# Kernel tuning notes

Hardware: AMD Instinct MI355X
Metric: run time of the kernel (lower is better)

The kernel has to match this reference:

```python
import jax, jax.numpy as jnp
import numpy as np

B = 2          # batch
S = 4096       # byte-level sequence length
D = 512        # d_hidden_bytelevel
BPL = 4        # bytes_per_latent
H = 16         # n_attention_heads
DQK = 64       # d_qkv_bytelevel (== rope d_hidden)
DLAT = 1024    # d_hidden_latent
LQ = S // BPL  # latent sequence length
EPS = 1.1920929e-07  # torch RMSNorm default eps = float32 finfo eps
ROPE_BASE = 10000.0


def _rope(x, pos):
    # x: [B, H, L, DQK], pos: [L] float positions. Half-split rotation.
    half = DQK // 2
    inv_freq = ROPE_BASE ** (-jnp.arange(half, dtype=jnp.float32) / half)  # [half]
    ang = pos[:, None] * inv_freq[None, :]                                 # [L, half]
    cos, sin = jnp.cos(ang), jnp.sin(ang)
    x1, x2 = x[..., :half], x[..., half:]
    return jnp.concatenate([x1 * cos - x2 * sin, x1 * sin + x2 * cos], axis=-1)


def setup_inputs() -> dict:
    key = jax.random.key(0)
    ks = jax.random.split(key, 9)
    s = 0.02
    return {
        "x": jax.random.normal(ks[0], (B, S, D), dtype=jnp.float32),
        "norm_w": jnp.ones((D,), dtype=jnp.float32),
        "wq_w": jax.random.normal(ks[1], (BPL * D, H * DQK), dtype=jnp.float32) * s,
        "wq_b": jax.random.normal(ks[2], (H * DQK,), dtype=jnp.float32) * s,
        "wkv_w": jax.random.normal(ks[3], (D, 2 * H * DQK), dtype=jnp.float32) * s,
        "wkv_b": jax.random.normal(ks[4], (2 * H * DQK,), dtype=jnp.float32) * s,
        "wout_w": jax.random.normal(ks[5], (H * DQK, DLAT), dtype=jnp.float32) * s,
        "wout_b": jax.random.normal(ks[6], (DLAT,), dtype=jnp.float32) * s,
        "wbyp_w": jax.random.normal(ks[7], (BPL * D, DLAT), dtype=jnp.float32) * s,
    }


def reference(x, norm_w, wq_w, wq_b, wkv_w, wkv_b, wout_w, wout_b, wbyp_w):
    # RMSNorm (elementwise affine)
    normalized = x * jax.lax.rsqrt(jnp.mean(x * x, axis=-1, keepdims=True) + EPS) * norm_w
    # merge groups of BPL bytes -> latent query tokens: [B, LQ, BPL*D]
    merged = normalized.reshape(B, LQ, BPL * D)
    # fused Q projection: [B, H, LQ, DQK]
    q = (merged @ wq_w + wq_b).reshape(B, LQ, H, DQK).transpose(0, 2, 1, 3)
    # merged KV projection: split dim first, then heads -> [B, S, 2, H, DQK]
    kv = (normalized @ wkv_w + wkv_b).reshape(B, S, 2, H, DQK)
    k = kv[:, :, 0].transpose(0, 2, 1, 3)  # [B, H, S, DQK]
    v = kv[:, :, 1].transpose(0, 2, 1, 3)
    # strided RoPE for Q (positions i*BPL), unit-stride for K
    q = _rope(q, jnp.arange(LQ, dtype=jnp.float32) * BPL)
    k = _rope(k, jnp.arange(S, dtype=jnp.float32))
    # SDPA (non-causal)
    scores = jnp.einsum('bhqd,bhkd->bhqk', q, k) * (1.0 / np.sqrt(DQK).astype(np.float32))
    attn = jax.nn.softmax(scores, axis=-1)
    attn_out = jnp.einsum('bhqk,bhkd->bhqd', attn, v)
    attn_concat = attn_out.transpose(0, 2, 1, 3).reshape(B, LQ, H * DQK)
    out = attn_concat @ wout_w + wout_b
    # bypass: raw x grouped by BPL, bias-free projection
    bypass = x.reshape(B, LQ, BPL * D) @ wbyp_w
    return out + bypass
```

## Files before the change

kernel.cpp:

```cpp
#include <hip/hip_runtime.h>

using u16 = unsigned short;
using u32 = unsigned int;

typedef __attribute__((ext_vector_type(8))) short bf16x8;
typedef __attribute__((ext_vector_type(8))) unsigned short u16x8;
typedef __attribute__((ext_vector_type(4))) float f32x4;
typedef __attribute__((ext_vector_type(16))) float f32x16;
typedef __attribute__((ext_vector_type(4))) u32 u32x4;

constexpr int Bb   = 2;
constexpr int Ss   = 4096;
constexpr int Dd   = 512;
constexpr int Hh   = 16;
constexpr int DQK  = 64;
constexpr int LQ   = 1024;
constexpr int DLAT = 1024;

#define QSCL 0.18033688011112042f

__device__ __forceinline__ u16 f2bf(float f){
  u32 u = __float_as_uint(f);
  u += 0x7FFFu + ((u >> 16) & 1u);
  return (u16)(u >> 16);
}
__device__ __forceinline__ u32 permpack(float hi, float lo){
  return __builtin_amdgcn_perm(__float_as_uint(hi), __float_as_uint(lo), 0x07060302u);
}

#define GLDS16(gp, lp) \
  __builtin_amdgcn_global_load_lds((const __attribute__((address_space(1))) u32*)(gp), \
                                   (__attribute__((address_space(3))) u32*)(lp), 16, 0, 0)

__global__ __launch_bounds__(256) void rmsnorm_kernel(
    const float* __restrict__ x, const float* __restrict__ w,
    u16* __restrict__ normb, u16* __restrict__ xb)
{
  const int lane = threadIdx.x & 63;
  const int row  = blockIdx.x * 4 + (threadIdx.x >> 6);
  const float4* xr = (const float4*)(x + (size_t)row * Dd);
  float4 a = xr[lane*2], b2 = xr[lane*2 + 1];
  float ss = a.x*a.x + a.y*a.y + a.z*a.z + a.w*a.w
           + b2.x*b2.x + b2.y*b2.y + b2.z*b2.z + b2.w*b2.w;
  #pragma unroll
  for (int off = 1; off < 64; off <<= 1) ss += __shfl_xor(ss, off);
  const float sc = rsqrtf(ss * (1.0f / Dd) + 1.1920929e-07f);
  const int c0 = lane * 8;
  const float4* wr4 = (const float4*)(w + c0);
  float4 w0 = wr4[0], w1 = wr4[1];
  u16x8 nv, xv;
  nv[0]=f2bf(a.x *sc*w0.x); nv[1]=f2bf(a.y *sc*w0.y); nv[2]=f2bf(a.z *sc*w0.z); nv[3]=f2bf(a.w *sc*w0.w);
  nv[4]=f2bf(b2.x*sc*w1.x); nv[5]=f2bf(b2.y*sc*w1.y); nv[6]=f2bf(b2.z*sc*w1.z); nv[7]=f2bf(b2.w*sc*w1.w);
  xv[0]=f2bf(a.x);  xv[1]=f2bf(a.y);  xv[2]=f2bf(a.z);  xv[3]=f2bf(a.w);
  xv[4]=f2bf(b2.x); xv[5]=f2bf(b2.y); xv[6]=f2bf(b2.z); xv[7]=f2bf(b2.w);
  *(u16x8*)(normb + (size_t)row * Dd + c0) = nv;
  *(u16x8*)(xb    + (size_t)row * Dd + c0) = xv;
}

__global__ __launch_bounds__(256) void rope_tab_kernel(float2* __restrict__ tab){
  int i = blockIdx.x * 256 + threadIdx.x;
  int pos = i >> 5, d = i & 31;
  float inv = exp2f(-(float)d * 0.41524101186092028f);
  float ang = (float)pos * inv;
  float s, c;
  sincosf(ang, &s, &c);
  tab[i] = make_float2(c, s);
}

__global__ __launch_bounds__(256) void transpose_cast_kernel(
    const float* __restrict__ W, u16* __restrict__ Wt,
    int N, int ldt, int koff)
{
  __shared__ float t[64][65];
  const int k0 = blockIdx.x * 64, n0 = blockIdx.y * 64;
  const int c = threadIdx.x & 63, r0 = threadIdx.x >> 6;
  #pragma unroll
  for (int i = 0; i < 16; ++i){
    int r = i*4 + r0;
    t[r][c] = W[(size_t)(k0 + r) * N + n0 + c];
  }
  __syncthreads();
  #pragma unroll
  for (int i = 0; i < 16; ++i){
    int r = i*4 + r0;
    Wt[(size_t)(n0 + r) * ldt + koff + k0 + c] = f2bf(t[c][r]);
  }
}

__device__ __forceinline__ void gemm_core64(
    const u16* __restrict__ A, int lda,
    const u16* __restrict__ Bt, int ldb, int kofs,
    int K, int bm0, int bn0, char* lds,
    f32x4 (&acc)[4])
{
  const int tid = threadIdx.x, lane = tid & 63, w = tid >> 6;
  const int l15 = lane & 15, l4 = lane >> 4;

  #pragma unroll
  for (int j = 0; j < 4; ++j) acc[j] = (f32x4){0.f, 0.f, 0.f, 0.f};

  auto stage = [&](int t){
    char* dst = lds + (t % 3) * 16384;
    const int k0 = t * 64;
    #pragma unroll
    for (int i = 0; i < 4; ++i){
      int u = i*256 + tid;
      int row = u >> 3;
      int colb = ((u & 7) * 16) ^ ((row & 7) << 4);
      const u16* src = (row < 64)
        ? A  + (size_t)(bm0 + row) * lda + k0 + (colb >> 1)
        : Bt + (size_t)(bn0 + row - 64) * ldb + kofs + k0 + (colb >> 1);
      GLDS16(src, dst + u*16);
    }
  };

  const int nt = K >> 6;
  stage(0);
  if (nt > 1) stage(1);

  #pragma unroll 1
  for (int t = 0; t < nt; ++t){
    if (t + 1 < nt) { asm volatile("s_waitcnt vmcnt(4)" ::: "memory"); }
    else            { asm volatile("s_waitcnt vmcnt(0)" ::: "memory"); }
    __builtin_amdgcn_sched_barrier(0);
    __builtin_amdgcn_s_barrier();

    const char* kb = lds + (t % 3) * 16384;
    bf16x8 af[2], bf[4][2];
    #pragma unroll
    for (int ks = 0; ks < 2; ++ks){
      const int row = w*16 + l15;
      af[ks] = *(const bf16x8*)(kb + row*128 + ((ks*64 + l4*16) ^ ((row & 7) << 4)));
    }
    #pragma unroll
    for (int j = 0; j < 4; ++j)
      #pragma unroll
      for (int ks = 0; ks < 2; ++ks){
        const int row = 64 + j*16 + l15;
        bf[j][ks] = *(const bf16x8*)(kb + row*128 + ((ks*64 + l4*16) ^ ((row & 7) << 4)));
      }
    asm volatile("s_waitcnt lgkmcnt(0)" ::: "memory");
    __builtin_amdgcn_sched_barrier(0);
    if (t + 2 < nt) stage(t + 2);

    __builtin_amdgcn_s_setprio(1);
    #pragma unroll
    for (int ks = 0; ks < 2; ++ks)
      #pragma unroll
      for (int j = 0; j < 4; ++j)
        acc[j] = __builtin_amdgcn_mfma_f32_16x16x32_bf16(af[ks], bf[j][ks], acc[j], 0, 0, 0);
    __builtin_amdgcn_s_setprio(0);
  }
}

__global__ __launch_bounds__(256, 3) void qkv_kernel(
    const u16* __restrict__ normb,
    const u16* __restrict__ wtq, const u16* __restrict__ wtkv,
    const float* __restrict__ wq_b, const float* __restrict__ wkv_b,
    const float2* __restrict__ rtab,
    u16* __restrict__ Qb, u16* __restrict__ Kb, u16* __restrict__ Vtb)
{
  __shared__ char lds[49152];
  const int bid = blockIdx.x;
  const int lane = threadIdx.x & 63, w = threadIdx.x >> 6;
  const int ml = (lane >> 4) * 4, nl = lane & 15;
  f32x4 acc[4];

  if (bid < 512){
    const int bm0 = (bid & 31) * 64, bn0 = (bid >> 5) * 64;
    gemm_core64(normb, 2048, wtq, 2048, 0, 2048, bm0, bn0, lds, acc);
    const int h = bn0 >> 6;
    #pragma unroll
    for (int j = 0; j < 2; ++j){
      const int d1 = j*16 + nl;
      const float b1 = wq_b[bn0 + j*16 + nl], b2v = wq_b[bn0 + (j+2)*16 + nl];
      #pragma unroll
      for (int r = 0; r < 4; ++r){
        int m = bm0 + w*16 + ml + r;
        int b = m >> 10, lq = m & 1023;
        float x1 = acc[j][r] + b1;
        float x2 = acc[j+2][r] + b2v;
        float2 cs = rtab[(lq*4)*32 + d1];
        size_t ob = ((size_t)(b*Hh + h) * LQ + lq) * DQK;
        Qb[ob + d1]      = f2bf((x1*cs.x - x2*cs.y) * QSCL);
        Qb[ob + d1 + 32] = f2bf((x1*cs.y + x2*cs.x) * QSCL);
      }
    }
  } else {
    const int t = bid - 512;
    const int bm0 = (t & 127) * 64, bn0 = (t >> 7) * 64;
    gemm_core64(normb, 512, wtkv, 512, 0, 512, bm0, bn0, lds, acc);
    const int kv = bn0 >> 10;
    const int h = (bn0 & 1023) >> 6;
    const int m0 = bm0 + w*16 + ml;
    const int b = m0 >> 12, s = m0 & 4095;
    if (kv == 0){
      #pragma unroll
      for (int r = 0; r < 4; ++r){
        size_t ob = ((size_t)(b*Hh + h) * Ss + s + r) * DQK;
        #pragma unroll
        for (int j = 0; j < 2; ++j){
          int d1 = j*16 + nl;
          float x1 = acc[j][r]   + wkv_b[bn0 + j*16 + nl];
          float x2 = acc[j+2][r] + wkv_b[bn0 + (j+2)*16 + nl];
          float2 cs = rtab[(s+r)*32 + d1];
          Kb[ob + d1]      = f2bf(x1*cs.x - x2*cs.y);
          Kb[ob + d1 + 32] = f2bf(x1*cs.y + x2*cs.x);
        }
      }
    } else {
      #pragma unroll
      for (int j = 0; j < 4; ++j){
        const int d = j*16 + nl;
        const float bb = wkv_b[bn0 + d];
        uint2 pv;
        pv.x = permpack(acc[j][1] + bb, acc[j][0] + bb);
        pv.y = permpack(acc[j][3] + bb, acc[j][2] + bb);
        *(uint2*)(Vtb + (((size_t)(b*Hh + h)) * DQK + d) * Ss + s) = pv;
      }
    }
  }
}

__global__ __launch_bounds__(256, 3) void out_kernel(
    const u16* __restrict__ ACb, const u16* __restrict__ xb,
    const u16* __restrict__ wto, const float* __restrict__ wout_b,
    float* __restrict__ outp)
{
  __shared__ char lds[49152];
  const int bm0 = blockIdx.x * 64, bn0 = blockIdx.y * 64;
  const int lane = threadIdx.x & 63, w = threadIdx.x >> 6;
  const int ml = (lane >> 4) * 4, nl = lane & 15;
  f32x4 acc[4], acc2[4];
  gemm_core64(ACb, 1024, wto, 3072, 0,    1024, bm0, bn0, lds, acc);
  __syncthreads();
  gemm_core64(xb,  2048, wto, 3072, 1024, 2048, bm0, bn0, lds, acc2);
  #pragma unroll
  for (int j = 0; j < 4; ++j){
    const int n = bn0 + j*16 + nl;
    const float bb = wout_b[n];
    #pragma unroll
    for (int r = 0; r < 4; ++r){
      int m = bm0 + w*16 + ml + r;
      outp[(size_t)m * DLAT + n] = acc[j][r] + acc2[j][r] + bb;
    }
  }
}

__global__ __launch_bounds__(512, 2) void flash_kernel(
    const u16* __restrict__ Qg, const u16* __restrict__ Kg,
    const u16* __restrict__ Vtg, float* __restrict__ Opart,
    float* __restrict__ lpart)
{
  const int tid = threadIdx.x, lane = tid & 63, w = tid >> 6;
  const int bid = blockIdx.x;
  const int swz = (bid & 7) * 32 + (bid >> 3);
  const int qt4 = swz & 3, half = (swz >> 2) & 1, bh = swz >> 3;
  const int q0 = qt4 * 256;
  const int sbase = half * 2048;
  const int l31 = lane & 31, hgl = lane >> 5;

  __shared__ char lds[49152];

  bf16x8 qf[4];
  #pragma unroll
  for (int ks = 0; ks < 4; ++ks)
    qf[ks] = *(const bf16x8*)(Qg + ((size_t)bh*LQ + q0 + w*32 + l31) * DQK + ks*16 + hgl*8);

  f32x16 o[2];
  #pragma unroll
  for (int nd = 0; nd < 2; ++nd)
    #pragma unroll
    for (int r = 0; r < 16; ++r) o[nd][r] = 0.f;
  float l_run = 0.f;

  auto stage = [&](int t){
    char* dst = lds + (t % 3) * 16384;
    const int s0 = sbase + t * 64;
    #pragma unroll
    for (int i = 0; i < 2; ++i){
      int u = (w*2 + i) * 64 + lane;
      int row = (u >> 3) & 63;
      int colb = ((u & 7) * 16) ^ ((row & 7) << 4);
      const u16* src = (u < 512)
          ? Kg  + ((size_t)bh*Ss  + s0 + row) * DQK + (colb >> 1)
          : Vtg + ((size_t)bh*DQK + row) * Ss + s0  + (colb >> 1);
      GLDS16(src, dst + u*16);
    }
  };

  stage(0);
  stage(1);

  #pragma unroll 1
  for (int t = 0; t < 32; ++t){
    if (t < 31) { asm volatile("s_waitcnt vmcnt(2)" ::: "memory"); }
    else        { asm volatile("s_waitcnt vmcnt(0)" ::: "memory"); }
    __builtin_amdgcn_sched_barrier(0);
    __builtin_amdgcn_s_barrier();

    const char* kb = lds + (t % 3) * 16384;
    bf16x8 kf[2][4], vf[2][4];
    #pragma unroll
    for (int kvt = 0; kvt < 2; ++kvt)
      #pragma unroll
      for (int ks = 0; ks < 4; ++ks){
        const int row = kvt*32 + l31;
        kf[kvt][ks] = *(const bf16x8*)(kb + row*128 + ((ks*32 + hgl*16) ^ ((row & 7) << 4)));
      }
    #pragma unroll
    for (int nd = 0; nd < 2; ++nd)
      #pragma unroll
      for (int k2 = 0; k2 < 4; ++k2){
        const int row = nd*32 + l31;
        vf[nd][k2] = *(const bf16x8*)(kb + 8192 + row*128 + ((k2*32 + hgl*16) ^ ((row & 7) << 4)));
      }
    asm volatile("s_waitcnt lgkmcnt(0)" ::: "memory");
    __builtin_amdgcn_sched_barrier(0);
    if (t < 30) stage(t + 2);

    f32x16 sc[2];
    #pragma unroll
    for (int kvt = 0; kvt < 2; ++kvt)
      #pragma unroll
      for (int r = 0; r < 16; ++r) sc[kvt][r] = 0.f;
    __builtin_amdgcn_s_setprio(1);
    #pragma unroll
    for (int kvt = 0; kvt < 2; ++kvt)
      #pragma unroll
      for (int ks = 0; ks < 4; ++ks)
        sc[kvt] = __builtin_amdgcn_mfma_f32_32x32x16_bf16(kf[kvt][ks], qf[ks], sc[kvt], 0, 0, 0);
    __builtin_amdgcn_s_setprio(0);

    float s_loc = 0.f;
    u32x4 paw[4];
    #pragma unroll
    for (int kvt = 0; kvt < 2; ++kvt){
      #pragma unroll
      for (int r = 0; r < 16; ++r){
        float p = __builtin_amdgcn_exp2f(sc[kvt][r]);
        sc[kvt][r] = p;
        s_loc += p;
      }
      #pragma unroll
      for (int k2r = 0; k2r < 2; ++k2r){
        u32 a0 = permpack(sc[kvt][k2r*8+1], sc[kvt][k2r*8+0]);
        u32 a1 = permpack(sc[kvt][k2r*8+3], sc[kvt][k2r*8+2]);
        u32 a2 = permpack(sc[kvt][k2r*8+5], sc[kvt][k2r*8+4]);
        u32 a3 = permpack(sc[kvt][k2r*8+7], sc[kvt][k2r*8+6]);
        asm("v_permlane32_swap_b32 %0, %1" : "+v"(a0), "+v"(a2));
        asm("v_permlane32_swap_b32 %0, %1" : "+v"(a1), "+v"(a3));
        const int k2 = kvt*2 + k2r;
        paw[k2][0] = a0; paw[k2][1] = a1;
        paw[k2][2] = a2; paw[k2][3] = a3;
      }
    }
    l_run += s_loc;

    __builtin_amdgcn_s_setprio(1);
    #pragma unroll
    for (int nd = 0; nd < 2; ++nd)
      #pragma unroll
      for (int k2 = 0; k2 < 4; ++k2)
        o[nd] = __builtin_amdgcn_mfma_f32_32x32x16_bf16(
            __builtin_bit_cast(bf16x8, paw[k2]), vf[nd][k2], o[nd], 0, 0, 0);
    __builtin_amdgcn_s_setprio(0);
  }

  float lf = l_run + __shfl_xor(l_run, 32);
  float* Ob = Opart + ((size_t)half * 32768 + (size_t)(bh*4 + qt4) * 256) * 64;
  #pragma unroll
  for (int nd = 0; nd < 2; ++nd)
    #pragma unroll
    for (int r = 0; r < 16; ++r){
      int q = w*32 + (r & 3) + 8*(r >> 2) + 4*hgl;
      Ob[(size_t)q * 64 + nd*32 + l31] = o[nd][r];
    }
  if (hgl == 0)
    lpart[(size_t)half * 32768 + (size_t)(bh*4 + qt4) * 256 + w*32 + l31] = lf;
}

__global__ __launch_bounds__(256) void merge_kernel(
    const float* __restrict__ Opart, const float* __restrict__ lpart,
    u16* __restrict__ AC)
{
  int idx = blockIdx.x * 256 + threadIdx.x;
  int row = idx >> 3, dg = idx & 7;
  int bh = row >> 10, lq = row & 1023;
  int b = bh >> 4, h = bh & 15;
  const float4* p0 = (const float4*)(Opart + (size_t)row * 64 + dg * 8);
  const float4* p1 = (const float4*)(Opart + ((size_t)32768 + row) * 64 + dg * 8);
  float4 a0 = p0[0], a1 = p0[1], c0 = p1[0], c1 = p1[1];
  float rl = 1.0f / (lpart[row] + lpart[32768 + row]);
  u16x8 r;
  r[0]=f2bf((a0.x+c0.x)*rl); r[1]=f2bf((a0.y+c0.y)*rl);
  r[2]=f2bf((a0.z+c0.z)*rl); r[3]=f2bf((a0.w+c0.w)*rl);
  r[4]=f2bf((a1.x+c1.x)*rl); r[5]=f2bf((a1.y+c1.y)*rl);
  r[6]=f2bf((a1.z+c1.z)*rl); r[7]=f2bf((a1.w+c1.w)*rl);
  *(u16x8*)(AC + ((size_t)(b*LQ + lq)) * (Hh*DQK) + h*DQK + dg*8) = r;
}

extern "C" void kernel_launch(void* const* d_in, const int* in_sizes, int n_in,
                              void* d_out, int out_size, void* d_ws, size_t ws_size,
                              hipStream_t stream)
{
  (void)in_sizes; (void)n_in; (void)out_size; (void)ws_size;
  const float* x      = (const float*)d_in[0];
  const float* norm_w = (const float*)d_in[1];
  const float* wq_w   = (const float*)d_in[2];
  const float* wq_b   = (const float*)d_in[3];
  const float* wkv_w  = (const float*)d_in[4];
  const float* wkv_b  = (const float*)d_in[5];
  const float* wout_w = (const float*)d_in[6];
  const float* wout_b = (const float*)d_in[7];
  const float* wbyp_w = (const float*)d_in[8];
  float* outp = (float*)d_out;

  char* p = (char*)d_ws;
  u16* normb = (u16*)p; p += (size_t)8192*512*2;
  u16* xb    = (u16*)p; p += (size_t)8192*512*2;
  u16* wtq   = (u16*)p; p += (size_t)1024*2048*2;
  u16* wtkv  = (u16*)p; p += (size_t)2048*512*2;
  u16* wto   = (u16*)p; p += (size_t)1024*3072*2;
  u16* Qb    = (u16*)p; p += (size_t)32*1024*64*2;
  u16* Kb    = (u16*)p; p += (size_t)32*4096*64*2;
  u16* Vtb   = (u16*)p; p += (size_t)32*64*4096*2;
  u16* ACb   = (u16*)p; p += (size_t)2048*1024*2;
  float2* rtab = (float2*)p; p += (size_t)4096*32*sizeof(float2);
  float* Opart = (float*)p; p += (size_t)2*32768*64*4;
  float* lpart = (float*)p; p += (size_t)2*32768*4;

  rmsnorm_kernel<<<2048, 256, 0, stream>>>(x, norm_w, normb, xb);
  rope_tab_kernel<<<512, 256, 0, stream>>>(rtab);
  transpose_cast_kernel<<<dim3(32,16), 256, 0, stream>>>(wq_w,   wtq,  1024, 2048, 0);
  transpose_cast_kernel<<<dim3(8,32),  256, 0, stream>>>(wkv_w,  wtkv, 2048, 512,  0);
  transpose_cast_kernel<<<dim3(16,16), 256, 0, stream>>>(wout_w, wto,  1024, 3072, 0);
  transpose_cast_kernel<<<dim3(32,16), 256, 0, stream>>>(wbyp_w, wto,  1024, 3072, 1024);

  qkv_kernel<<<4608, 256, 0, stream>>>(normb, wtq, wtkv, wq_b, wkv_b, rtab, Qb, Kb, Vtb);
  flash_kernel<<<256, 512, 0, stream>>>(Qb, Kb, Vtb, Opart, lpart);
  merge_kernel<<<1024, 256, 0, stream>>>(Opart, lpart, ACb);
  out_kernel<<<dim3(32,16), 256, 0, stream>>>(ACb, xb, wto, wout_b, outp);
}
```

Baseline: 143.4 us.

## Double Q rows per wave and split KV four ways in flash kernel

Each wave now processes two 32-row Q tiles against every staged K/V tile, which halves K/V LDS reads and global loads per unit of work. To keep the block count fixed, the KV sequence is split into four chunks instead of two, and the merge kernel sums four partials. This raises register pressure from the doubled Q fragments and accumulators, and doubles the partial-output traffic written and read by the merge step.

```diff
diff --git a/kernel.cpp b/kernel.cpp
--- a/kernel.cpp
+++ b/kernel.cpp
@@ -255,24 +255,27 @@
   const int tid = threadIdx.x, lane = tid & 63, w = tid >> 6;
   const int bid = blockIdx.x;
   const int swz = (bid & 7) * 32 + (bid >> 3);
-  const int qt4 = swz & 3, half = (swz >> 2) & 1, bh = swz >> 3;
-  const int q0 = qt4 * 256;
-  const int sbase = half * 2048;
+  const int sq = swz & 3, qh = (swz >> 2) & 1, bh = swz >> 3;
+  const int sbase = sq * 1024;
   const int l31 = lane & 31, hgl = lane >> 5;
 
   __shared__ char lds[49152];
 
-  bf16x8 qf[4];
-  #pragma unroll
-  for (int ks = 0; ks < 4; ++ks)
-    qf[ks] = *(const bf16x8*)(Qg + ((size_t)bh*LQ + q0 + w*32 + l31) * DQK + ks*16 + hgl*8);
-
-  f32x16 o[2];
-  #pragma unroll
-  for (int nd = 0; nd < 2; ++nd)
-    #pragma unroll
-    for (int r = 0; r < 16; ++r) o[nd][r] = 0.f;
-  float l_run = 0.f;
+  bf16x8 qf[2][4];
+  #pragma unroll
+  for (int qt = 0; qt < 2; ++qt)
+    #pragma unroll
+    for (int ks = 0; ks < 4; ++ks)
+      qf[qt][ks] = *(const bf16x8*)(Qg + ((size_t)bh*LQ + qh*512 + w*64 + qt*32 + l31) * DQK + ks*16 + hgl*8);
+
+  f32x16 o[2][2];
+  #pragma unroll
+  for (int qt = 0; qt < 2; ++qt)
+    #pragma unroll
+    for (int nd = 0; nd < 2; ++nd)
+      #pragma unroll
+      for (int r = 0; r < 16; ++r) o[qt][nd][r] = 0.f;
+  float l_run[2] = {0.f, 0.f};
 
   auto stage = [&](int t){
     char* dst = lds + (t % 3) * 16384;
@@ -293,8 +296,8 @@
   stage(1);
 
   #pragma unroll 1
-  for (int t = 0; t < 32; ++t){
-    if (t < 31) { asm volatile("s_waitcnt vmcnt(2)" ::: "memory"); }
+  for (int t = 0; t < 16; ++t){
+    if (t < 15) { asm volatile("s_waitcnt vmcnt(2)" ::: "memory"); }
     else        { asm volatile("s_waitcnt vmcnt(0)" ::: "memory"); }
     __builtin_amdgcn_sched_barrier(0);
     __builtin_amdgcn_s_barrier();
@@ -317,67 +320,73 @@
       }
     asm volatile("s_waitcnt lgkmcnt(0)" ::: "memory");
     __builtin_amdgcn_sched_barrier(0);
-    if (t < 30) stage(t + 2);
-
-    f32x16 sc[2];
-    #pragma unroll
-    for (int kvt = 0; kvt < 2; ++kvt)
-      #pragma unroll
-      for (int r = 0; r < 16; ++r) sc[kvt][r] = 0.f;
-    __builtin_amdgcn_s_setprio(1);
-    #pragma unroll
-    for (int kvt = 0; kvt < 2; ++kvt)
-      #pragma unroll
-      for (int ks = 0; ks < 4; ++ks)
-        sc[kvt] = __builtin_amdgcn_mfma_f32_32x32x16_bf16(kf[kvt][ks], qf[ks], sc[kvt], 0, 0, 0);
-    __builtin_amdgcn_s_setprio(0);
-
-    float s_loc = 0.f;
-    u32x4 paw[4];
-    #pragma unroll
-    for (int kvt = 0; kvt < 2; ++kvt){
+    if (t < 14) stage(t + 2);
+
+    #pragma unroll
+    for (int qt = 0; qt < 2; ++qt){
+      f32x16 sc[2];
+      #pragma unroll
+      for (int kvt = 0; kvt < 2; ++kvt)
+        #pragma unroll
+        for (int r = 0; r < 16; ++r) sc[kvt][r] = 0.f;
+      __builtin_amdgcn_s_setprio(1);
+      #pragma unroll
+      for (int kvt = 0; kvt < 2; ++kvt)
+        #pragma unroll
+        for (int ks = 0; ks < 4; ++ks)
+          sc[kvt] = __builtin_amdgcn_mfma_f32_32x32x16_bf16(kf[kvt][ks], qf[qt][ks], sc[kvt], 0, 0, 0);
+      __builtin_amdgcn_s_setprio(0);
+
+      float s_loc = 0.f;
+      u32x4 paw[4];
+      #pragma unroll
+      for (int kvt = 0; kvt < 2; ++kvt){
+        #pragma unroll
+        for (int r = 0; r < 16; ++r){
+          float p = __builtin_amdgcn_exp2f(sc[kvt][r]);
+          sc[kvt][r] = p;
+          s_loc += p;
+        }
+        #pragma unroll
+        for (int k2r = 0; k2r < 2; ++k2r){
+          u32 a0 = permpack(sc[kvt][k2r*8+1], sc[kvt][k2r*8+0]);
+          u32 a1 = permpack(sc[kvt][k2r*8+3], sc[kvt][k2r*8+2]);
+          u32 a2 = permpack(sc[kvt][k2r*8+5], sc[kvt][k2r*8+4]);
+          u32 a3 = permpack(sc[kvt][k2r*8+7], sc[kvt][k2r*8+6]);
+          asm("v_permlane32_swap_b32 %0, %1" : "+v"(a0), "+v"(a2));
+          asm("v_permlane32_swap_b32 %0, %1" : "+v"(a1), "+v"(a3));
+          const int k2 = kvt*2 + k2r;
+          paw[k2][0] = a0; paw[k2][1] = a1;
+          paw[k2][2] = a2; paw[k2][3] = a3;
+        }
+      }
+      l_run[qt] += s_loc;
+
+      __builtin_amdgcn_s_setprio(1);
+      #pragma unroll
+      for (int nd = 0; nd < 2; ++nd)
+        #pragma unroll
+        for (int k2 = 0; k2 < 4; ++k2)
+          o[qt][nd] = __builtin_amdgcn_mfma_f32_32x32x16_bf16(
+              __builtin_bit_cast(bf16x8, paw[k2]), vf[nd][k2], o[qt][nd], 0, 0, 0);
+      __builtin_amdgcn_s_setprio(0);
+    }
+  }
+
+  #pragma unroll
+  for (int qt = 0; qt < 2; ++qt){
+    float lf = l_run[qt] + __shfl_xor(l_run[qt], 32);
+    float* Ob = Opart + ((size_t)sq * 32768 + (size_t)bh * 1024) * 64;
+    #pragma unroll
+    for (int nd = 0; nd < 2; ++nd)
       #pragma unroll
       for (int r = 0; r < 16; ++r){
-        float p = __builtin_amdgcn_exp2f(sc[kvt][r]);
-        sc[kvt][r] = p;
-        s_loc += p;
-      }
-      #pragma unroll
-      for (int k2r = 0; k2r < 2; ++k2r){
-        u32 a0 = permpack(sc[kvt][k2r*8+1], sc[kvt][k2r*8+0]);
-        u32 a1 = permpack(sc[kvt][k2r*8+3], sc[kvt][k2r*8+2]);
-        u32 a2 = permpack(sc[kvt][k2r*8+5], sc[kvt][k2r*8+4]);
-        u32 a3 = permpack(sc[kvt][k2r*8+7], sc[kvt][k2r*8+6]);
-        asm("v_permlane32_swap_b32 %0, %1" : "+v"(a0), "+v"(a2));
-        asm("v_permlane32_swap_b32 %0, %1" : "+v"(a1), "+v"(a3));
-        const int k2 = kvt*2 + k2r;
-        paw[k2][0] = a0; paw[k2][1] = a1;
-        paw[k2][2] = a2; paw[k2][3] = a3;
-      }
-    }
-    l_run += s_loc;
-
-    __builtin_amdgcn_s_setprio(1);
-    #pragma unroll
-    for (int nd = 0; nd < 2; ++nd)
-      #pragma unroll
-      for (int k2 = 0; k2 < 4; ++k2)
-        o[nd] = __builtin_amdgcn_mfma_f32_32x32x16_bf16(
-            __builtin_bit_cast(bf16x8, paw[k2]), vf[nd][k2], o[nd], 0, 0, 0);
-    __builtin_amdgcn_s_setprio(0);
-  }
-
-  float lf = l_run + __shfl_xor(l_run, 32);
-  float* Ob = Opart + ((size_t)half * 32768 + (size_t)(bh*4 + qt4) * 256) * 64;
-  #pragma unroll
-  for (int nd = 0; nd < 2; ++nd)
-    #pragma unroll
-    for (int r = 0; r < 16; ++r){
-      int q = w*32 + (r & 3) + 8*(r >> 2) + 4*hgl;
-      Ob[(size_t)q * 64 + nd*32 + l31] = o[nd][r];
-    }
-  if (hgl == 0)
-    lpart[(size_t)half * 32768 + (size_t)(bh*4 + qt4) * 256 + w*32 + l31] = lf;
+        int q = qh*512 + w*64 + qt*32 + (r & 3) + 8*(r >> 2) + 4*hgl;
+        Ob[(size_t)q * 64 + nd*32 + l31] = o[qt][nd][r];
+      }
+    if (hgl == 0)
+      lpart[(size_t)sq * 32768 + (size_t)bh * 1024 + qh*512 + w*64 + qt*32 + l31] = lf;
+  }
 }
 
 __global__ __launch_bounds__(256) void merge_kernel(
@@ -388,15 +397,22 @@
   int row = idx >> 3, dg = idx & 7;
   int bh = row >> 10, lq = row & 1023;
   int b = bh >> 4, h = bh & 15;
-  const float4* p0 = (const float4*)(Opart + (size_t)row * 64 + dg * 8);
-  const float4* p1 = (const float4*)(Opart + ((size_t)32768 + row) * 64 + dg * 8);
-  float4 a0 = p0[0], a1 = p0[1], c0 = p1[0], c1 = p1[1];
-  float rl = 1.0f / (lpart[row] + lpart[32768 + row]);
+  float a[8];
+  #pragma unroll
+  for (int e = 0; e < 8; ++e) a[e] = 0.f;
+  float lt = 0.f;
+  #pragma unroll
+  for (int p = 0; p < 4; ++p){
+    const float4* pp = (const float4*)(Opart + ((size_t)p * 32768 + row) * 64 + dg * 8);
+    float4 v0 = pp[0], v1 = pp[1];
+    a[0]+=v0.x; a[1]+=v0.y; a[2]+=v0.z; a[3]+=v0.w;
+    a[4]+=v1.x; a[5]+=v1.y; a[6]+=v1.z; a[7]+=v1.w;
+    lt += lpart[(size_t)p * 32768 + row];
+  }
+  float rl = 1.0f / lt;
   u16x8 r;
-  r[0]=f2bf((a0.x+c0.x)*rl); r[1]=f2bf((a0.y+c0.y)*rl);
-  r[2]=f2bf((a0.z+c0.z)*rl); r[3]=f2bf((a0.w+c0.w)*rl);
-  r[4]=f2bf((a1.x+c1.x)*rl); r[5]=f2bf((a1.y+c1.y)*rl);
-  r[6]=f2bf((a1.z+c1.z)*rl); r[7]=f2bf((a1.w+c1.w)*rl);
+  #pragma unroll
+  for (int e = 0; e < 8; ++e) r[e] = f2bf(a[e] * rl);
   *(u16x8*)(AC + ((size_t)(b*LQ + lq)) * (Hh*DQK) + h*DQK + dg*8) = r;
 }
 
@@ -427,8 +443,8 @@
   u16* Vtb   = (u16*)p; p += (size_t)32*64*4096*2;
   u16* ACb   = (u16*)p; p += (size_t)2048*1024*2;
   float2* rtab = (float2*)p; p += (size_t)4096*32*sizeof(float2);
-  float* Opart = (float*)p; p += (size_t)2*32768*64*4;
-  float* lpart = (float*)p; p += (size_t)2*32768*4;
+  float* Opart = (float*)p; p += (size_t)4*32768*64*4;
+  float* lpart = (float*)p; p += (size_t)4*32768*4;
 
   rmsnorm_kernel<<<2048, 256, 0, stream>>>(x, norm_w, normb, xb);
   rope_tab_kernel<<<512, 256, 0, stream>>>(rtab);
```

After: 137.7 us. 3.9% less time.
